# Optimization experiments

Measured on AMD Instinct MI355X. Metric: run time of the kernel, lower is better.

## Reference

```python
import jax, jax.numpy as jnp
import numpy as np

N = 100000   # nodes
E = 1600000  # edges
G = 64       # graphs in batch
F_IN = 128
H = 128
SV = 64
AD = 32


def setup_inputs() -> dict:
    key = jax.random.key(0)
    ks = jax.random.split(key, 12)
    s = 0.05
    return {
        "x": jax.random.normal(ks[0], (N, F_IN), jnp.float32),
        "edge_index": jax.random.randint(ks[1], (2, E), 0, N, dtype=jnp.int64),
        "batch": jnp.sort(jax.random.randint(ks[2], (N,), 0, G, dtype=jnp.int64)),
        "state_vector": jax.random.normal(ks[3], (G, SV), jnp.float32),
        "action": jax.random.normal(ks[4], (G, AD), jnp.float32),
        "W1": jax.random.normal(ks[5], (F_IN, H), jnp.float32) * s,
        "b1": jnp.zeros((H,), jnp.float32),
        "W2": jax.random.normal(ks[6], (H, H), jnp.float32) * s,
        "b2": jnp.zeros((H,), jnp.float32),
        "Wf1": jax.random.normal(ks[7], (H + SV + AD, 256), jnp.float32) * s,
        "bf1": jnp.zeros((256,), jnp.float32),
        "Wf2": jax.random.normal(ks[8], (256, 256), jnp.float32) * s,
        "bf2": jnp.zeros((256,), jnp.float32),
        "Wo": jax.random.normal(ks[9], (256, 1), jnp.float32) * s,
        "bo": jnp.zeros((1,), jnp.float32),
    }


def gcn_conv(x, W, b, src, dst, deg_inv_sqrt):
    # PyG GCNConv: h = x @ W; aggregate D^-1/2 (A+I) D^-1/2 h; + b
    h = x @ W
    norm = deg_inv_sqrt[src] * deg_inv_sqrt[dst]          # [E]
    agg = jax.ops.segment_sum(h[src] * norm[:, None], dst, num_segments=N)
    agg = agg + h * (deg_inv_sqrt * deg_inv_sqrt)[:, None]  # self loops
    return agg + b


def reference(x, edge_index, batch, state_vector, action,
              W1, b1, W2, b2, Wf1, bf1, Wf2, bf2, Wo, bo):
    src, dst = edge_index[0], edge_index[1]
    # degree after adding self loops (aggregation index = dst, PyG default flow)
    deg = jax.ops.segment_sum(jnp.ones((E,), jnp.float32), dst, num_segments=N) + 1.0
    deg_inv_sqrt = jax.lax.rsqrt(deg)

    h = jax.nn.relu(gcn_conv(x, W1, b1, src, dst, deg_inv_sqrt))
    h = jax.nn.relu(gcn_conv(h, W2, b2, src, dst, deg_inv_sqrt))

    # global_mean_pool over graph ids
    sums = jax.ops.segment_sum(h, batch, num_segments=G)
    cnts = jax.ops.segment_sum(jnp.ones((N,), jnp.float32), batch, num_segments=G)
    pooled = sums / jnp.maximum(cnts, 1.0)[:, None]       # [G, H]

    z = jnp.concatenate([pooled, state_vector, action], axis=1)  # [G, H+SV+AD]
    z = jax.nn.relu(z @ Wf1 + bf1)
    z = jax.nn.relu(z @ Wf2 + bf2)
    return z @ Wo + bo                                     # [G, 1]
```

## Files before the change

### kernel.cpp

```cpp
#include <hip/hip_runtime.h>
#include <hip/hip_bf16.h>
#include <stdint.h>

#define N_NODES 100000
#define N_EDGES 1600000
#define N_GRAPHS 64
#define HDIM 128

#define BUCKET_SHIFT 9
#define NBUCK ((N_NODES + 511) >> 9)
#define CAP 9728
#define SCAT_CHUNK 8192
#define SCAT_NBLK ((N_EDGES + SCAT_CHUNK - 1) / SCAT_CHUNK)
#define GB_NBLK ((N_NODES + 255) / 256)
#define NPB ((N_NODES + 7) / 8)
#define RED_CHUNKS 8

typedef __bf16 bf16x8 __attribute__((ext_vector_type(8)));
typedef float f32x4 __attribute__((ext_vector_type(4)));
typedef float f32x2 __attribute__((ext_vector_type(2)));

__global__ __launch_bounds__(256) void setup_kernel(const int* __restrict__ batch,
                                                    int* __restrict__ gstart,
                                                    const float* __restrict__ W1,
                                                    const float* __restrict__ W2,
                                                    __hip_bfloat16* __restrict__ Wt1,
                                                    __hip_bfloat16* __restrict__ Wt2,
                                                    int* __restrict__ gcur,
                                                    float* __restrict__ psum0) {
    int bid = blockIdx.x;
    if (bid < GB_NBLK) {
        int i = bid * 256 + threadIdx.x;
        if (i >= N_NODES) return;
        int b = batch[i];
        int prev = (i == 0) ? -1 : batch[i - 1];
        for (int g = prev + 1; g <= b; ++g) gstart[g] = i;
        if (i == N_NODES - 1) {
            for (int g = b + 1; g <= N_GRAPHS; ++g) gstart[g] = N_NODES;
        }
    } else if (bid < GB_NBLK + 128) {
        int t = bid - GB_NBLK;
        const float* W = (t < 64) ? W1 : W2;
        __hip_bfloat16* Wt = (t < 64) ? Wt1 : Wt2;
        int bb = t & 63;
        int n = bb * 2 + (threadIdx.x >> 7);
        int k = threadIdx.x & 127;
        Wt[n * 128 + k] = __float2bfloat16(W[k * 128 + n]);
    } else {
        int i = (bid - GB_NBLK - 128) * 256 + threadIdx.x;
        if (i < NBUCK) gcur[i] = i * CAP;
        int j = i - NBUCK;
        if (j >= 0 && j < N_GRAPHS * HDIM) psum0[j] = 0.f;
    }
}
#define SETUP_NBLK (GB_NBLK + 128 + (NBUCK + N_GRAPHS * HDIM + 255) / 256)

__global__ __launch_bounds__(256) void scatter_kernel(const int* __restrict__ src,
                                                      const int* __restrict__ dst,
                                                      int* __restrict__ gcur,
                                                      int* __restrict__ sorted, int E) {
    __shared__ int hist[NBUCK];
    __shared__ int base_s[NBUCK];
    int tid = threadIdx.x;
    int e0 = blockIdx.x * SCAT_CHUNK;
    int sv[SCAT_CHUNK / 256], dv[SCAT_CHUNK / 256];
#pragma unroll
    for (int j = 0; j < SCAT_CHUNK / 256; j++) {
        int e = e0 + (j << 8) + tid;
        if (e < E) { sv[j] = src[e]; dv[j] = dst[e]; } else { sv[j] = -1; dv[j] = -1; }
    }
    if (tid < NBUCK) hist[tid] = 0;
    __syncthreads();
#pragma unroll
    for (int j = 0; j < SCAT_CHUNK / 256; j++)
        if (dv[j] >= 0) atomicAdd(&hist[dv[j] >> BUCKET_SHIFT], 1);
    __syncthreads();
    if (tid < NBUCK) {
        int c = hist[tid];
        base_s[tid] = (c > 0) ? atomicAdd(&gcur[tid], c) : 0;
    }
    __syncthreads();
    if (tid < NBUCK) hist[tid] = 0;
    __syncthreads();
#pragma unroll
    for (int j = 0; j < SCAT_CHUNK / 256; j++) {
        if (dv[j] >= 0) {
            int b = dv[j] >> BUCKET_SHIFT;
            int idx = atomicAdd(&hist[b], 1);
            sorted[base_s[b] + idx] = ((dv[j] & 511) << 17) | sv[j];
        }
    }
}

__global__ __launch_bounds__(256) void bucket_build_kernel(const int* __restrict__ sorted,
                                                           const int* __restrict__ gcur,
                                                           int2* __restrict__ rs2,
                                                           float* __restrict__ dis,
                                                           int* __restrict__ csr_src) {
    __shared__ int edges[CAP];
    __shared__ int cnt[512];
    __shared__ int excl[512];
    __shared__ int ps[256];
    int b = blockIdx.x, tid = threadIdx.x;
    cnt[tid] = 0; cnt[tid + 256] = 0;
    int node0 = b << BUCKET_SHIFT;
    int lo = b * CAP, hi = gcur[b];
    int ne = hi - lo;
    for (int i = tid; i < ne; i += 256) edges[i] = sorted[lo + i];
    __syncthreads();
    for (int i = tid; i < ne; i += 256)
        atomicAdd(&cnt[((unsigned)edges[i]) >> 17], 1);
    __syncthreads();
    int c0 = cnt[2 * tid], c1 = cnt[2 * tid + 1];
    ps[tid] = c0 + c1;
    __syncthreads();
#pragma unroll
    for (int off = 1; off < 256; off <<= 1) {
        int t = (tid >= off) ? ps[tid - off] : 0;
        __syncthreads();
        ps[tid] += t;
        __syncthreads();
    }
    int pex = ps[tid] - (c0 + c1);
    excl[2 * tid] = pex;
    excl[2 * tid + 1] = pex + c0;
    __syncthreads();
#pragma unroll
    for (int k = 0; k < 2; k++) {
        int li = tid + k * 256;
        int node = node0 + li;
        if (node < N_NODES) {
            int st = lo + excl[li] + li;
            int c = cnt[li];
            rs2[node] = make_int2(st, st + c + 1);
            dis[node] = rsqrtf((float)c + 1.0f);
            csr_src[st + c] = node;
        }
    }
    cnt[tid] = 0; cnt[tid + 256] = 0;
    __syncthreads();
    for (int i = tid; i < ne; i += 256) {
        int v = edges[i];
        int li = ((unsigned)v) >> 17;
        int idx = atomicAdd(&cnt[li], 1);
        csr_src[lo + excl[li] + li + idx] = v & 0x1FFFF;
    }
}

template<bool A_FP32>
__global__ __launch_bounds__(256) void gemm_mfma_kernel(const void* __restrict__ Av,
                                                        const __hip_bfloat16* __restrict__ Wt,
                                                        const float* __restrict__ scale,
                                                        unsigned char* __restrict__ C, int nrows) {
    __shared__ float Cs[64 * 132];
    int tid = threadIdx.x;
    int wave = tid >> 6, lane = tid & 63;
    int quad = lane >> 4, l16 = lane & 15;
    int row0 = blockIdx.x * 64;
    int arow = row0 + wave * 16 + l16;
    int arow_c = min(arow, nrows - 1);

    const __hip_bfloat16* A16 = (const __hip_bfloat16*)Av;
    const float* A32 = (const float*)Av;

    f32x4 acc[8];
#pragma unroll
    for (int t = 0; t < 8; t++) acc[t] = (f32x4){0.f, 0.f, 0.f, 0.f};

#pragma unroll
    for (int kt = 0; kt < 4; kt++) {
        int kbase = kt * 32 + quad * 8;
        union { bf16x8 v; __hip_bfloat16 h[8]; uint4 u; } au;
        if (A_FP32) {
            const float* ap = A32 + (size_t)arow_c * 128 + kbase;
            float4 u0 = *(const float4*)ap;
            float4 u1 = *(const float4*)(ap + 4);
            au.h[0] = __float2bfloat16(u0.x); au.h[1] = __float2bfloat16(u0.y);
            au.h[2] = __float2bfloat16(u0.z); au.h[3] = __float2bfloat16(u0.w);
            au.h[4] = __float2bfloat16(u1.x); au.h[5] = __float2bfloat16(u1.y);
            au.h[6] = __float2bfloat16(u1.z); au.h[7] = __float2bfloat16(u1.w);
        } else {
            au.u = *(const uint4*)(A16 + (size_t)arow_c * 128 + kbase);
        }
#pragma unroll
        for (int t = 0; t < 8; t++) {
            bf16x8 b = *(const bf16x8*)(Wt + (size_t)(t * 16 + l16) * 128 + kbase);
            acc[t] = __builtin_amdgcn_mfma_f32_16x16x32_bf16(au.v, b, acc[t], 0, 0, 0);
        }
    }

    int rbase = wave * 16 + quad * 4;
    float s[4];
#pragma unroll
    for (int r = 0; r < 4; r++) s[r] = scale[min(row0 + rbase + r, nrows - 1)];
#pragma unroll
    for (int t = 0; t < 8; t++) {
#pragma unroll
        for (int r = 0; r < 4; r++)
            Cs[(rbase + r) * 132 + t * 16 + l16] = acc[t][r] * s[r];
    }
    __syncthreads();

#pragma unroll
    for (int p = 0; p < 4; p++) {
        int g = p * 256 + tid;
        int row = g >> 4, c8 = (g & 15) * 8;
        int grow = row0 + row;
        if (grow < nrows) {
            const float* cp = &Cs[row * 132 + c8];
            float4 v0 = *(const float4*)cp;
            float4 v1 = *(const float4*)(cp + 4);
            int w0 = __builtin_amdgcn_cvt_pk_fp8_f32(v0.x, v0.y, 0, false);
            w0 = __builtin_amdgcn_cvt_pk_fp8_f32(v0.z, v0.w, w0, true);
            int w1 = __builtin_amdgcn_cvt_pk_fp8_f32(v1.x, v1.y, 0, false);
            w1 = __builtin_amdgcn_cvt_pk_fp8_f32(v1.z, v1.w, w1, true);
            *(uint2*)(C + (size_t)grow * 128 + c8) = make_uint2((unsigned)w0, (unsigned)w1);
        }
    }
}

__device__ __forceinline__ void accum8p(f32x2* acc, uint2 u) {
    acc[0] += __builtin_amdgcn_cvt_pk_f32_fp8((int)u.x, false);
    acc[1] += __builtin_amdgcn_cvt_pk_f32_fp8((int)u.x, true);
    acc[2] += __builtin_amdgcn_cvt_pk_f32_fp8((int)u.y, false);
    acc[3] += __builtin_amdgcn_cvt_pk_f32_fp8((int)u.y, true);
}

template<bool FUSE_POOL>
__global__ __launch_bounds__(256, 8) void agg_kernel(const unsigned char* __restrict__ h8,
                                                     const float* __restrict__ dis,
                                                     const int2* __restrict__ rs2,
                                                     const int* __restrict__ csr_src,
                                                     const float* __restrict__ bias,
                                                     __hip_bfloat16* __restrict__ out,
                                                     const int* __restrict__ batch,
                                                     float* __restrict__ pp,
                                                     float* __restrict__ psum0, int n) {
    __shared__ float psum_s[512];
    int tid = threadIdx.x;
    int wid = tid >> 6;
    int lane = tid & 63;
    int half = lane >> 5;
    int q = lane >> 4;
    int f = lane & 15;
    int l32 = lane & 31;
    int sub = q & 1;
    int hb = half << 5;
    unsigned fo = (unsigned)(f * 8);
    int blk0 = (int)blockIdx.x * 8;

    if (FUSE_POOL) {
        psum_s[tid] = 0.f; psum_s[tid + 256] = 0.f;
        __syncthreads();
    }

    int nodeA = blk0 + wid * 2;
    bool active = nodeA < n;
    if (!FUSE_POOL && !active) return;
    int nodeB = nodeA + 1;
    bool hasB = nodeB < n;
    int myNode = half ? (hasB ? nodeB : nodeA) : nodeA;
    myNode = min(myNode, n - 1);

    int2 se = rs2[myNode];
    int i0 = se.x;
    int deg = se.y - se.x;
    if ((half && !hasB) || !active) deg = 0;
    float dn = dis[myNode];

    f32x2 acc[4];
#pragma unroll
    for (int j = 0; j < 4; j++) acc[j] = (f32x2){0.f, 0.f};

    for (int base = 0; base < deg; base += 32) {
        int cnt = min(deg - base, 32);
        int idx = csr_src[i0 + base + min(l32, cnt - 1)];
        int e = 0;
        for (; e + 16 <= cnt; e += 16) {
            int s0 = __shfl(idx, hb + e + sub, 64);
            int s1 = __shfl(idx, hb + e + 2 + sub, 64);
            int s2 = __shfl(idx, hb + e + 4 + sub, 64);
            int s3 = __shfl(idx, hb + e + 6 + sub, 64);
            int s4 = __shfl(idx, hb + e + 8 + sub, 64);
            int s5 = __shfl(idx, hb + e + 10 + sub, 64);
            int s6 = __shfl(idx, hb + e + 12 + sub, 64);
            int s7 = __shfl(idx, hb + e + 14 + sub, 64);
            uint2 u0 = *(const uint2*)(h8 + (unsigned)(s0 << 7) + fo);
            uint2 u1 = *(const uint2*)(h8 + (unsigned)(s1 << 7) + fo);
            uint2 u2 = *(const uint2*)(h8 + (unsigned)(s2 << 7) + fo);
            uint2 u3 = *(const uint2*)(h8 + (unsigned)(s3 << 7) + fo);
            uint2 u4 = *(const uint2*)(h8 + (unsigned)(s4 << 7) + fo);
            uint2 u5 = *(const uint2*)(h8 + (unsigned)(s5 << 7) + fo);
            uint2 u6 = *(const uint2*)(h8 + (unsigned)(s6 << 7) + fo);
            uint2 u7 = *(const uint2*)(h8 + (unsigned)(s7 << 7) + fo);
            accum8p(acc, u0);
            accum8p(acc, u1);
            accum8p(acc, u2);
            accum8p(acc, u3);
            accum8p(acc, u4);
            accum8p(acc, u5);
            accum8p(acc, u6);
            accum8p(acc, u7);
        }
        if (e < cnt) {
            int r = cnt - 1;
#pragma unroll
            for (int k = 0; k < 8; k++) {
                int ln = e + 2 * k + sub;
                int s = __shfl(idx, hb + min(ln, r), 64);
                uint2 u = *(const uint2*)(h8 + (unsigned)(s << 7) + fo);
                if (ln > r) { u.x = 0u; u.y = 0u; }
                accum8p(acc, u);
            }
        }
    }

#pragma unroll
    for (int j = 0; j < 4; j++) {
        f32x2 v = acc[j];
        v[0] += __shfl_down(v[0], 16, 64);
        v[1] += __shfl_down(v[1], 16, 64);
        acc[j] = v;
    }

    bool res = active && (sub == 0) && (half == 0 || hasB);

    if (FUSE_POOL) {
        float rv[8];
        {
            float4 b0 = *(const float4*)(bias + f * 8);
            float4 b1 = *(const float4*)(bias + f * 8 + 4);
            float bb[8] = {b0.x, b0.y, b0.z, b0.w, b1.x, b1.y, b1.z, b1.w};
#pragma unroll
            for (int k = 0; k < 4; k++) {
                rv[2 * k]     = fmaxf(fmaf(acc[k][0], dn, bb[2 * k]), 0.f);
                rv[2 * k + 1] = fmaxf(fmaf(acc[k][1], dn, bb[2 * k + 1]), 0.f);
            }
        }
        int gA = batch[blk0];
        int gB = batch[min(blk0 + 7, n - 1)];
        if (gA == gB) {
#pragma unroll
            for (int k = 0; k < 8; k++) rv[k] += __shfl_down(rv[k], 32, 64);
            if (lane < 16 && active) {
#pragma unroll
                for (int k = 0; k < 8; k++) psum_s[wid * 128 + f * 8 + k] = rv[k];
            }
            __syncthreads();
            if (tid < 128) {
                float v = psum_s[tid] + psum_s[128 + tid] + psum_s[256 + tid] + psum_s[384 + tid];
                pp[(size_t)blockIdx.x * 128 + tid] = v;
            }
        } else {
            if (res) {
                int g = batch[myNode];
#pragma unroll
                for (int k = 0; k < 8; k++)
                    atomicAdd(&psum0[g * 128 + f * 8 + k], rv[k]);
            }
        }
    } else {
        if (res) {
            float4 b0 = *(const float4*)(bias + f * 8);
            float4 b1 = *(const float4*)(bias + f * 8 + 4);
            float r0 = fmaxf(fmaf(acc[0][0], dn, b0.x), 0.f);
            float r1 = fmaxf(fmaf(acc[0][1], dn, b0.y), 0.f);
            float r2 = fmaxf(fmaf(acc[1][0], dn, b0.z), 0.f);
            float r3 = fmaxf(fmaf(acc[1][1], dn, b0.w), 0.f);
            float r4 = fmaxf(fmaf(acc[2][0], dn, b1.x), 0.f);
            float r5 = fmaxf(fmaf(acc[2][1], dn, b1.y), 0.f);
            float r6 = fmaxf(fmaf(acc[3][0], dn, b1.z), 0.f);
            float r7 = fmaxf(fmaf(acc[3][1], dn, b1.w), 0.f);
            __hip_bfloat162 p0 = __float22bfloat162_rn(make_float2(r0, r1));
            __hip_bfloat162 p1 = __float22bfloat162_rn(make_float2(r2, r3));
            __hip_bfloat162 p2 = __float22bfloat162_rn(make_float2(r4, r5));
            __hip_bfloat162 p3 = __float22bfloat162_rn(make_float2(r6, r7));
            uint4 pk;
            pk.x = *(unsigned int*)&p0; pk.y = *(unsigned int*)&p1;
            pk.z = *(unsigned int*)&p2; pk.w = *(unsigned int*)&p3;
            *(uint4*)(out + (size_t)myNode * 128 + f * 8) = pk;
        }
    }
}

__global__ __launch_bounds__(256) void pool_reduce_kernel(const float* __restrict__ pp,
                                                          const int* __restrict__ gstart,
                                                          float* __restrict__ pp2) {
    __shared__ float red[256];
    int r = blockIdx.x;
    int g = r >> 3, c = r & (RED_CHUNKS - 1);
    int lo = gstart[g], hi = gstart[g + 1];
    int b_lo = (lo + 7) >> 3;
    int b_hi = hi >> 3;
    int nb = b_hi - b_lo;
    int per = (nb + RED_CHUNKS - 1) >> 3;
    int r0 = b_lo + c * per;
    int r1 = min(b_hi, r0 + per);
    int feat = threadIdx.x & 127;
    int sg = threadIdx.x >> 7;
    float s = 0.f;
    for (int b = r0 + sg; b < r1; b += 2)
        s += pp[(size_t)b * 128 + feat];
    red[threadIdx.x] = s;
    __syncthreads();
    if (threadIdx.x < 128)
        pp2[(size_t)r * 128 + threadIdx.x] = red[threadIdx.x] + red[threadIdx.x + 128];
}

__global__ __launch_bounds__(256) void mlp_kernel(const float* __restrict__ pp2,
                                                  const float* __restrict__ psum0,
                                                  const int* __restrict__ gstart,
                                                  const float* __restrict__ sv,
                                                  const float* __restrict__ act,
                                                  const float* __restrict__ Wf1,
                                                  const float* __restrict__ bf1,
                                                  const float* __restrict__ Wf2,
                                                  const float* __restrict__ bf2,
                                                  const float* __restrict__ Wo,
                                                  const float* __restrict__ bo,
                                                  float* __restrict__ out) {
    int g = blockIdx.x, tid = threadIdx.x;
    __shared__ float z[224];
    __shared__ float z1[256];
    __shared__ float red[256];
    int lo = gstart[g], hi = gstart[g + 1];
    if (tid < 128) {
        float s = psum0[g * 128 + tid];
#pragma unroll
        for (int c = 0; c < RED_CHUNKS; c++)
            s += pp2[(size_t)(g * RED_CHUNKS + c) * 128 + tid];
        float cnt = fmaxf((float)(hi - lo), 1.f);
        z[tid] = s / cnt;
    } else if (tid < 192) {
        z[tid] = sv[g * 64 + (tid - 128)];
    } else if (tid < 224) {
        z[tid] = act[g * 32 + (tid - 192)];
    }
    __syncthreads();
    float a = bf1[tid];
    for (int k = 0; k < 224; k++) a = fmaf(z[k], Wf1[k * 256 + tid], a);
    z1[tid] = fmaxf(a, 0.f);
    __syncthreads();
    float b = bf2[tid];
    for (int k = 0; k < 256; k++) b = fmaf(z1[k], Wf2[k * 256 + tid], b);
    b = fmaxf(b, 0.f);
    red[tid] = b * Wo[tid];
    __syncthreads();
    for (int off = 128; off > 0; off >>= 1) {
        if (tid < off) red[tid] += red[tid + off];
        __syncthreads();
    }
    if (tid == 0) out[g] = red[0] + bo[0];
}

extern "C" void kernel_launch(void* const* d_in, const int* in_sizes, int n_in,
                              void* d_out, int out_size, void* d_ws, size_t ws_size,
                              hipStream_t stream) {
    const float* x   = (const float*)d_in[0];
    const int*   eidx = (const int*)d_in[1];
    const int*   batch = (const int*)d_in[2];
    const float* sv  = (const float*)d_in[3];
    const float* act = (const float*)d_in[4];
    const float* W1  = (const float*)d_in[5];
    const float* b1  = (const float*)d_in[6];
    const float* W2  = (const float*)d_in[7];
    const float* b2  = (const float*)d_in[8];
    const float* Wf1 = (const float*)d_in[9];
    const float* bf1 = (const float*)d_in[10];
    const float* Wf2 = (const float*)d_in[11];
    const float* bf2 = (const float*)d_in[12];
    const float* Wo  = (const float*)d_in[13];
    const float* bo  = (const float*)d_in[14];
    float* out = (float*)d_out;

    const int* srcp = eidx;
    const int* dstp = eidx + N_EDGES;

    char* w = (char*)d_ws;
    int* gcur = (int*)w;               w += (size_t)NBUCK * 4;
    int2* rs2 = (int2*)w;              w += (size_t)N_NODES * 8;
    float* dis = (float*)w;            w += (size_t)N_NODES * 4;
    int* gstart = (int*)w;             w += (size_t)(N_GRAPHS + 1) * 4;
    w = (char*)(((uintptr_t)w + 255) & ~(uintptr_t)255);
    float* pp = (float*)w;             w += (size_t)NPB * HDIM * 4;
    float* pp2 = (float*)w;            w += (size_t)N_GRAPHS * RED_CHUNKS * HDIM * 4;
    float* psum0 = (float*)w;          w += (size_t)N_GRAPHS * HDIM * 4;
    w = (char*)(((uintptr_t)w + 255) & ~(uintptr_t)255);
    int* csr_src = (int*)w;            w += (size_t)NBUCK * CAP * 4;
    w = (char*)(((uintptr_t)w + 255) & ~(uintptr_t)255);
    int* sorted = (int*)w;             w += (size_t)NBUCK * CAP * 4;
    w = (char*)(((uintptr_t)w + 255) & ~(uintptr_t)255);
    __hip_bfloat16* Wt1 = (__hip_bfloat16*)w;   w += (size_t)HDIM * HDIM * 2;
    __hip_bfloat16* Wt2 = (__hip_bfloat16*)w;   w += (size_t)HDIM * HDIM * 2;
    w = (char*)(((uintptr_t)w + 255) & ~(uintptr_t)255);
    unsigned char* hbuf = (unsigned char*)w;    w += (size_t)N_NODES * HDIM;
    w = (char*)(((uintptr_t)w + 255) & ~(uintptr_t)255);
    __hip_bfloat16* abuf = (__hip_bfloat16*)w;  w += (size_t)N_NODES * HDIM * 2;

    setup_kernel<<<SETUP_NBLK, 256, 0, stream>>>(batch, gstart, W1, W2, Wt1, Wt2, gcur, psum0);

    scatter_kernel<<<SCAT_NBLK, 256, 0, stream>>>(srcp, dstp, gcur, sorted, N_EDGES);
    bucket_build_kernel<<<NBUCK, 256, 0, stream>>>(sorted, gcur, rs2, dis, csr_src);

    int gemm_blocks = (N_NODES + 63) / 64;

    gemm_mfma_kernel<true><<<gemm_blocks, 256, 0, stream>>>(x, Wt1, dis, hbuf, N_NODES);
    agg_kernel<false><<<NPB, 256, 0, stream>>>(hbuf, dis, rs2, csr_src, b1, abuf,
                                               batch, pp, psum0, N_NODES);
    gemm_mfma_kernel<false><<<gemm_blocks, 256, 0, stream>>>(abuf, Wt2, dis, hbuf, N_NODES);
    agg_kernel<true><<<NPB, 256, 0, stream>>>(hbuf, dis, rs2, csr_src, b2, abuf,
                                              batch, pp, psum0, N_NODES);

    pool_reduce_kernel<<<N_GRAPHS * RED_CHUNKS, 256, 0, stream>>>(pp, gstart, pp2);
    mlp_kernel<<<N_GRAPHS, 256, 0, stream>>>(pp2, psum0, gstart, sv, act,
                                             Wf1, bf1, Wf2, bf2, Wo, bo, out);
}
```

Measured before the change: 296.3 us.

## Fuse edge scatter with first GEMM and move source-degree scaling into aggregation

The GEMM no longer multiplies rows by deg^-1/2, so the first GEMM no longer depends on the CSR/degree build. It is merged into one launch with the edge scatter kernel, with block ranges split between the two jobs, so they can overlap and one launch is saved. The aggregation kernel now loads dis[src] per edge and broadcasts it via shuffles to scale each neighbor's contribution. This adds per-edge gathers and FMAs in the hot aggregation loop. Storing unscaled values in FP8 also changes the quantization behavior.

```diff
diff --git a/kernel.cpp b/kernel.cpp
--- a/kernel.cpp
+++ b/kernel.cpp
@@ -12,6 +12,7 @@
 #define CAP 9728
 #define SCAT_CHUNK 8192
 #define SCAT_NBLK ((N_EDGES + SCAT_CHUNK - 1) / SCAT_CHUNK)
+#define GEMM_NBLK ((N_NODES + 63) / 64)
 #define GB_NBLK ((N_NODES + 255) / 256)
 #define NPB ((N_NODES + 7) / 8)
 #define RED_CHUNKS 8
@@ -55,14 +56,13 @@
 }
 #define SETUP_NBLK (GB_NBLK + 128 + (NBUCK + N_GRAPHS * HDIM + 255) / 256)
 
-__global__ __launch_bounds__(256) void scatter_kernel(const int* __restrict__ src,
-                                                      const int* __restrict__ dst,
-                                                      int* __restrict__ gcur,
-                                                      int* __restrict__ sorted, int E) {
-    __shared__ int hist[NBUCK];
-    __shared__ int base_s[NBUCK];
+__device__ void scatter_body(const int* __restrict__ src,
+                             const int* __restrict__ dst,
+                             int* __restrict__ gcur,
+                             int* __restrict__ sorted, int E, int bid,
+                             int* hist, int* base_s) {
     int tid = threadIdx.x;
-    int e0 = blockIdx.x * SCAT_CHUNK;
+    int e0 = bid * SCAT_CHUNK;
     int sv[SCAT_CHUNK / 256], dv[SCAT_CHUNK / 256];
 #pragma unroll
     for (int j = 0; j < SCAT_CHUNK / 256; j++) {
@@ -148,15 +148,14 @@
 }
 
 template<bool A_FP32>
-__global__ __launch_bounds__(256) void gemm_mfma_kernel(const void* __restrict__ Av,
-                                                        const __hip_bfloat16* __restrict__ Wt,
-                                                        const float* __restrict__ scale,
-                                                        unsigned char* __restrict__ C, int nrows) {
-    __shared__ float Cs[64 * 132];
+__device__ void gemm_body(const void* __restrict__ Av,
+                          const __hip_bfloat16* __restrict__ Wt,
+                          unsigned char* __restrict__ C, int nrows, int bid,
+                          float* Cs ) {
     int tid = threadIdx.x;
     int wave = tid >> 6, lane = tid & 63;
     int quad = lane >> 4, l16 = lane & 15;
-    int row0 = blockIdx.x * 64;
+    int row0 = bid * 64;
     int arow = row0 + wave * 16 + l16;
     int arow_c = min(arow, nrows - 1);
 
@@ -190,14 +189,11 @@
     }
 
     int rbase = wave * 16 + quad * 4;
-    float s[4];
-#pragma unroll
-    for (int r = 0; r < 4; r++) s[r] = scale[min(row0 + rbase + r, nrows - 1)];
 #pragma unroll
     for (int t = 0; t < 8; t++) {
 #pragma unroll
         for (int r = 0; r < 4; r++)
-            Cs[(rbase + r) * 132 + t * 16 + l16] = acc[t][r] * s[r];
+            Cs[(rbase + r) * 132 + t * 16 + l16] = acc[t][r];
     }
     __syncthreads();
 
@@ -219,11 +215,35 @@
     }
 }
 
-__device__ __forceinline__ void accum8p(f32x2* acc, uint2 u) {
-    acc[0] += __builtin_amdgcn_cvt_pk_f32_fp8((int)u.x, false);
-    acc[1] += __builtin_amdgcn_cvt_pk_f32_fp8((int)u.x, true);
-    acc[2] += __builtin_amdgcn_cvt_pk_f32_fp8((int)u.y, false);
-    acc[3] += __builtin_amdgcn_cvt_pk_f32_fp8((int)u.y, true);
+__global__ __launch_bounds__(256) void scatter_gemm1_kernel(const int* __restrict__ src,
+                                                            const int* __restrict__ dst,
+                                                            int* __restrict__ gcur,
+                                                            int* __restrict__ sorted,
+                                                            const float* __restrict__ x,
+                                                            const __hip_bfloat16* __restrict__ Wt1,
+                                                            unsigned char* __restrict__ hbuf) {
+    __shared__ float Cs[64 * 132];
+    if (blockIdx.x < SCAT_NBLK) {
+        scatter_body(src, dst, gcur, sorted, N_EDGES, blockIdx.x,
+                     (int*)Cs, (int*)Cs + NBUCK);
+    } else {
+        gemm_body<true>(x, Wt1, hbuf, N_NODES, blockIdx.x - SCAT_NBLK, Cs);
+    }
+}
+
+__global__ __launch_bounds__(256) void gemm_mfma_kernel(const void* __restrict__ Av,
+                                                        const __hip_bfloat16* __restrict__ Wt,
+                                                        unsigned char* __restrict__ C, int nrows) {
+    __shared__ float Cs[64 * 132];
+    gemm_body<false>(Av, Wt, C, nrows, blockIdx.x, Cs);
+}
+
+__device__ __forceinline__ void accum8pf(f32x2* acc, uint2 u, float d) {
+    f32x2 dd = {d, d};
+    acc[0] += dd * __builtin_amdgcn_cvt_pk_f32_fp8((int)u.x, false);
+    acc[1] += dd * __builtin_amdgcn_cvt_pk_f32_fp8((int)u.x, true);
+    acc[2] += dd * __builtin_amdgcn_cvt_pk_f32_fp8((int)u.y, false);
+    acc[3] += dd * __builtin_amdgcn_cvt_pk_f32_fp8((int)u.y, true);
 }
 
 template<bool FUSE_POOL>
@@ -275,6 +295,7 @@
     for (int base = 0; base < deg; base += 32) {
         int cnt = min(deg - base, 32);
         int idx = csr_src[i0 + base + min(l32, cnt - 1)];
+        float dsv = dis[idx];
         int e = 0;
         for (; e + 16 <= cnt; e += 16) {
             int s0 = __shfl(idx, hb + e + sub, 64);
@@ -293,24 +314,34 @@
             uint2 u5 = *(const uint2*)(h8 + (unsigned)(s5 << 7) + fo);
             uint2 u6 = *(const uint2*)(h8 + (unsigned)(s6 << 7) + fo);
             uint2 u7 = *(const uint2*)(h8 + (unsigned)(s7 << 7) + fo);
-            accum8p(acc, u0);
-            accum8p(acc, u1);
-            accum8p(acc, u2);
-            accum8p(acc, u3);
-            accum8p(acc, u4);
-            accum8p(acc, u5);
-            accum8p(acc, u6);
-            accum8p(acc, u7);
+            float d0 = __shfl(dsv, hb + e + sub, 64);
+            float d1 = __shfl(dsv, hb + e + 2 + sub, 64);
+            float d2 = __shfl(dsv, hb + e + 4 + sub, 64);
+            float d3 = __shfl(dsv, hb + e + 6 + sub, 64);
+            float d4 = __shfl(dsv, hb + e + 8 + sub, 64);
+            float d5 = __shfl(dsv, hb + e + 10 + sub, 64);
+            float d6 = __shfl(dsv, hb + e + 12 + sub, 64);
+            float d7 = __shfl(dsv, hb + e + 14 + sub, 64);
+            accum8pf(acc, u0, d0);
+            accum8pf(acc, u1, d1);
+            accum8pf(acc, u2, d2);
+            accum8pf(acc, u3, d3);
+            accum8pf(acc, u4, d4);
+            accum8pf(acc, u5, d5);
+            accum8pf(acc, u6, d6);
+            accum8pf(acc, u7, d7);
         }
         if (e < cnt) {
             int r = cnt - 1;
 #pragma unroll
             for (int k = 0; k < 8; k++) {
                 int ln = e + 2 * k + sub;
-                int s = __shfl(idx, hb + min(ln, r), 64);
+                int sl = hb + min(ln, r);
+                int s = __shfl(idx, sl, 64);
+                float d = __shfl(dsv, sl, 64);
                 uint2 u = *(const uint2*)(h8 + (unsigned)(s << 7) + fo);
                 if (ln > r) { u.x = 0u; u.y = 0u; }
-                accum8p(acc, u);
+                accum8pf(acc, u, d);
             }
         }
     }
@@ -343,8 +374,8 @@
 #pragma unroll
             for (int k = 0; k < 8; k++) rv[k] += __shfl_down(rv[k], 32, 64);
             if (lane < 16 && active) {
-#pragma unroll
-                for (int k = 0; k < 8; k++) psum_s[wid * 128 + f * 8 + k] = rv[k];
+                *(float4*)&psum_s[wid * 128 + f * 8]     = make_float4(rv[0], rv[1], rv[2], rv[3]);
+                *(float4*)&psum_s[wid * 128 + f * 8 + 4] = make_float4(rv[4], rv[5], rv[6], rv[7]);
             }
             __syncthreads();
             if (tid < 128) {
@@ -499,15 +530,13 @@
 
     setup_kernel<<<SETUP_NBLK, 256, 0, stream>>>(batch, gstart, W1, W2, Wt1, Wt2, gcur, psum0);
 
-    scatter_kernel<<<SCAT_NBLK, 256, 0, stream>>>(srcp, dstp, gcur, sorted, N_EDGES);
+    scatter_gemm1_kernel<<<SCAT_NBLK + GEMM_NBLK, 256, 0, stream>>>(srcp, dstp, gcur, sorted,
+                                                                    x, Wt1, hbuf);
     bucket_build_kernel<<<NBUCK, 256, 0, stream>>>(sorted, gcur, rs2, dis, csr_src);
 
-    int gemm_blocks = (N_NODES + 63) / 64;
-
-    gemm_mfma_kernel<true><<<gemm_blocks, 256, 0, stream>>>(x, Wt1, dis, hbuf, N_NODES);
     agg_kernel<false><<<NPB, 256, 0, stream>>>(hbuf, dis, rs2, csr_src, b1, abuf,
                                                batch, pp, psum0, N_NODES);
-    gemm_mfma_kernel<false><<<gemm_blocks, 256, 0, stream>>>(abuf, Wt2, dis, hbuf, N_NODES);
+    gemm_mfma_kernel<<<GEMM_NBLK, 256, 0, stream>>>(abuf, Wt2, hbuf, N_NODES);
     agg_kernel<true><<<NPB, 256, 0, stream>>>(hbuf, dis, rs2, csr_src, b2, abuf,
                                               batch, pp, psum0, N_NODES);
 
```

Measured after the change: 314.3 us. 6.1% more time.
